# Kernel optimization log

Hardware: AMD Instinct MI355X
Metric: run time of the kernel (lower is better)

The kernel has to match this reference:

```python
import jax, jax.numpy as jnp
import numpy as np

N_NODES = 50000


def _gcn_conv(x, edge_index, W, b):
    """PyG-style GCNConv: add self-loops, symmetric deg^-1/2 norm, linear + scatter-add + bias."""
    n = x.shape[0]
    # add self loops
    loop = jnp.arange(n, dtype=edge_index.dtype)
    src = jnp.concatenate([edge_index[0], loop])  # [E+N]
    dst = jnp.concatenate([edge_index[1], loop])
    ones = jnp.ones_like(dst, dtype=x.dtype)
    deg = jax.ops.segment_sum(ones, dst, num_segments=n)  # in-degree incl. self loop
    deg_inv_sqrt = jnp.where(deg > 0, jax.lax.rsqrt(deg), 0.0)
    norm = deg_inv_sqrt[src] * deg_inv_sqrt[dst]  # [E+N]
    h = x @ W  # [N, out]
    msg = h[src] * norm[:, None]  # gather + scale, [E+N, out]
    out = jax.ops.segment_sum(msg, dst, num_segments=n)  # scatter-add
    return out + b


def setup_inputs() -> dict:
    key = jax.random.key(0)
    k1, k2, k3, k4 = jax.random.split(key, 4)
    in_ch, hid, z = 128, 128, 64
    x = jax.random.normal(k1, (N_NODES, in_ch), dtype=jnp.float32)
    edge_index = jax.random.randint(k2, (2, 800000), 0, N_NODES, dtype=jnp.int64)
    W1 = jax.random.normal(k3, (in_ch, hid), dtype=jnp.float32) * (1.0 / np.sqrt(in_ch))
    b1 = jnp.zeros((hid,), dtype=jnp.float32)
    W2 = jax.random.normal(k4, (hid, z), dtype=jnp.float32) * (1.0 / np.sqrt(hid))
    b2 = jnp.zeros((z,), dtype=jnp.float32)
    return {"x": x, "edge_index": edge_index, "W1": W1, "b1": b1, "W2": W2, "b2": b2}


def reference(x, edge_index, W1, b1, W2, b2):
    h = jax.nn.relu(_gcn_conv(x, edge_index, W1, b1))
    return _gcn_conv(h, edge_index, W2, b2)
```

## Files before the change

### kernel.cpp

```cpp
#include <hip/hip_runtime.h>

static constexpr int K = 128;
static constexpr int CAP = 8192;

using ushort8 = __attribute__((ext_vector_type(8))) unsigned short;
using bf16x8  = __attribute__((ext_vector_type(8))) __bf16;
using f32x4   = __attribute__((ext_vector_type(4))) float;

__device__ inline float bflo(unsigned u) { return __uint_as_float(u << 16); }
__device__ inline float bfhi(unsigned u) { return __uint_as_float(u & 0xFFFF0000u); }
__device__ inline unsigned short f2bf(float f) {
    unsigned u = __float_as_uint(f);
    return (unsigned short)((u + 0x7FFF + ((u >> 16) & 1)) >> 16);
}


__global__ __launch_bounds__(256) void k_bin(const int* __restrict__ ei, int e,
                                             int* __restrict__ gcur,
                                             unsigned long long* __restrict__ tmp) {
    constexpr int PER = 4;
    __shared__ int cnt[256], base[256], cur[256];
    int t = threadIdx.x;
    int chunk0 = blockIdx.x * 256 * PER;
    cnt[t] = 0;
    __syncthreads();
    int ds[PER];
#pragma unroll
    for (int k2 = 0; k2 < PER; ++k2) {
        int i = chunk0 + k2 * 256 + t;
        ds[k2] = (i < e) ? ei[(size_t)e + i] : -1;
        if (ds[k2] >= 0) atomicAdd(&cnt[ds[k2] >> 8], 1);
    }
    __syncthreads();
    int c = cnt[t];
    base[t] = c ? atomicAdd(&gcur[t], c) : 0;
    cur[t] = 0;
    __syncthreads();
#pragma unroll
    for (int k2 = 0; k2 < PER; ++k2) {
        int i = chunk0 + k2 * 256 + t;
        if (i < e) {
            int b = ds[k2] >> 8;
            int pos = base[b] + atomicAdd(&cur[b], 1);
            tmp[(size_t)b * CAP + pos] =
                ((unsigned long long)(unsigned)ds[k2] << 32) | (unsigned)ei[i];
        }
    }
}

__global__ __launch_bounds__(256) void k_bscan(const int* __restrict__ gcur,
                                               int* __restrict__ bbase,
                                               int nb, int* __restrict__ offs,
                                               int n, int e) {
    __shared__ int sh[256];
    int t = threadIdx.x;
    int v = (t < nb) ? gcur[t] : 0;
    sh[t] = v;
    __syncthreads();
    for (int o = 1; o < 256; o <<= 1) {
        int x = (t >= o) ? sh[t - o] : 0;
        __syncthreads();
        sh[t] += x;
        __syncthreads();
    }
    bbase[t] = sh[t] - v;
    if (t == 255) bbase[256] = sh[255];
    if (t == 0) offs[n] = e;
}

__global__ __launch_bounds__(1024) void k_csr(const unsigned long long* __restrict__ tmp,
                                              const int* __restrict__ bbase,
                                              int* __restrict__ offs,
                                              int* __restrict__ srt,
                                              float* __restrict__ dinv, int n) {
    __shared__ int cntS[256], sh[256], cur[256];
    int b = blockIdx.x;
    int t = threadIdx.x;
    int beg = bbase[b];
    int tot = bbase[b + 1] - beg;
    const unsigned long long* tb = tmp + (size_t)b * CAP;
    if (t < 256) cntS[t] = 0;
    __syncthreads();
    for (int i = t; i < tot; i += 1024)
        atomicAdd(&cntS[(int)(tb[i] >> 32) & 255], 1);
    __syncthreads();
    int v = (t < 256) ? cntS[t] : 0;
    if (t < 256) sh[t] = v;
    __syncthreads();
    for (int o = 1; o < 256; o <<= 1) {
        int x = (t < 256 && t >= o) ? sh[t - o] : 0;
        __syncthreads();
        if (t < 256) sh[t] += x;
        __syncthreads();
    }
    if (t < 256) {
        int pfx = sh[t] - v;
        int node = b * 256 + t;
        if (node < n) {
            offs[node] = beg + pfx;
            dinv[node] = rsqrtf((float)(v + 1));
        }
        cur[t] = pfx;
    }
    __syncthreads();
    for (int i = t; i < tot; i += 1024) {
        unsigned long long pr = tb[i];
        int d = (int)(pr >> 32);
        int pos = atomicAdd(&cur[d & 255], 1);
        srt[beg + pos] = (int)(pr & 0xFFFFFFFFu);
    }
}


template <int COUT>
__global__ __launch_bounds__(256) void k_gemm_mfma(const float* __restrict__ X,
                                                   const float* __restrict__ W,
                                                   const float* __restrict__ dinv,
                                                   unsigned short* __restrict__ G, int n) {
    constexpr int BM = 64, BK = 32;
    constexpr int NCT = COUT / 16;
    constexpr int NCH = K / BK;
    constexpr int WT = COUT * (BK / 8) / 256;
    __shared__ unsigned short Ah[BM * BK], Al[BM * BK];
    __shared__ unsigned short Bh[COUT * BK], Bl[COUT * BK];
    __shared__ float dS[BM];
    const int tid = threadIdx.x;
    const int row0 = blockIdx.x * BM;
    if (tid < BM) {
        int gr = row0 + tid;
        dS[tid] = (gr < n) ? dinv[gr] : 0.f;
    }

    float4 xr[2];
    float wr[WT][8];

    auto loadX = [&](int kc) {
        int r = tid >> 2, ks = tid & 3;
        int gr = row0 + r;
        if (gr < n) {
            const float4* pp = (const float4*)(X + (size_t)gr * K + kc * BK + ks * 8);
            xr[0] = pp[0];
            xr[1] = pp[1];
        } else {
            xr[0] = make_float4(0.f, 0.f, 0.f, 0.f);
            xr[1] = xr[0];
        }
    };
    auto loadW = [&](int kc) {
#pragma unroll
        for (int q = 0; q < WT; ++q) {
            int i = tid + q * 256;
            int c = i % COUT, ks = i / COUT;
#pragma unroll
            for (int j = 0; j < 8; ++j)
                wr[q][j] = W[(size_t)(kc * BK + ks * 8 + j) * COUT + c];
        }
    };
    auto storeLDS = [&]() {
        int r = tid >> 2, ks = tid & 3;
        ushort8 h, l;
        const float* f = (const float*)&xr[0];
#pragma unroll
        for (int j = 0; j < 8; ++j) {
            unsigned short hh = f2bf(f[j]);
            h[j] = hh;
            l[j] = f2bf(f[j] - __uint_as_float((unsigned)hh << 16));
        }
        *(ushort8*)&Ah[r * BK + ks * 8] = h;
        *(ushort8*)&Al[r * BK + ks * 8] = l;
#pragma unroll
        for (int q = 0; q < WT; ++q) {
            int i = tid + q * 256;
            int c = i % COUT, ks2 = i / COUT;
            ushort8 wh, wl;
#pragma unroll
            for (int j = 0; j < 8; ++j) {
                unsigned short hh = f2bf(wr[q][j]);
                wh[j] = hh;
                wl[j] = f2bf(wr[q][j] - __uint_as_float((unsigned)hh << 16));
            }
            *(ushort8*)&Bh[c * BK + ks2 * 8] = wh;
            *(ushort8*)&Bl[c * BK + ks2 * 8] = wl;
        }
    };

    f32x4 acc[NCT] = {};
    const int l = tid & 63, wv = tid >> 6;
    const int l16 = l & 15, lk = l >> 4;
    const int arow = wv * 16 + l16;

    loadX(0);
    loadW(0);
    storeLDS();
    __syncthreads();
    for (int c = 0; c < NCH; ++c) {
        if (c + 1 < NCH) { loadX(c + 1); loadW(c + 1); }
        bf16x8 ah = *(const bf16x8*)&Ah[arow * BK + lk * 8];
        bf16x8 al = *(const bf16x8*)&Al[arow * BK + lk * 8];
#pragma unroll
        for (int ct = 0; ct < NCT; ++ct) {
            bf16x8 bh = *(const bf16x8*)&Bh[(ct * 16 + l16) * BK + lk * 8];
            bf16x8 bl = *(const bf16x8*)&Bl[(ct * 16 + l16) * BK + lk * 8];
            acc[ct] = __builtin_amdgcn_mfma_f32_16x16x32_bf16(ah, bh, acc[ct], 0, 0, 0);
            acc[ct] = __builtin_amdgcn_mfma_f32_16x16x32_bf16(al, bh, acc[ct], 0, 0, 0);
            acc[ct] = __builtin_amdgcn_mfma_f32_16x16x32_bf16(ah, bl, acc[ct], 0, 0, 0);
        }
        if (c + 1 < NCH) {
            __syncthreads();
            storeLDS();
            __syncthreads();
        }
    }

#pragma unroll
    for (int ct = 0; ct < NCT; ++ct) {
        int col = ct * 16 + l16;
#pragma unroll
        for (int r4 = 0; r4 < 4; ++r4) {
            int lr = wv * 16 + lk * 4 + r4;
            int gr = row0 + lr;
            if (gr < n) G[(size_t)gr * COUT + col] = f2bf(acc[ct][r4] * dS[lr]);
        }
    }
}


__global__ __launch_bounds__(256) void k_gemm_bf16(const unsigned short* __restrict__ X,
                                                   const float* __restrict__ W,
                                                   const float* __restrict__ dinv,
                                                   unsigned short* __restrict__ G, int n) {
    constexpr int COUT = 64, BM = 64, BK = 32;
    constexpr int NCT = COUT / 16;
    constexpr int NCH = K / BK;
    __shared__ unsigned short Ah[BM * BK];
    __shared__ unsigned short Bh[COUT * BK], Bl[COUT * BK];
    __shared__ float dS[BM];
    const int tid = threadIdx.x;
    const int row0 = blockIdx.x * BM;
    if (tid < BM) {
        int gr = row0 + tid;
        dS[tid] = (gr < n) ? dinv[gr] : 0.f;
    }

    ushort8 xrb;
    float wr[8];

    auto loadX = [&](int kc) {
        int r = tid >> 2, ks = tid & 3;
        int gr = row0 + r;
        if (gr < n)
            xrb = *(const ushort8*)(X + (size_t)gr * K + kc * BK + ks * 8);
        else
            xrb = (ushort8){0, 0, 0, 0, 0, 0, 0, 0};
    };
    auto loadW = [&](int kc) {
        int c = tid % COUT, ks = tid / COUT;
#pragma unroll
        for (int j = 0; j < 8; ++j)
            wr[j] = W[(size_t)(kc * BK + ks * 8 + j) * COUT + c];
    };
    auto storeLDS = [&]() {
        int r = tid >> 2, ks = tid & 3;
        *(ushort8*)&Ah[r * BK + ks * 8] = xrb;
        int c = tid % COUT, ks2 = tid / COUT;
        ushort8 wh, wl;
#pragma unroll
        for (int j = 0; j < 8; ++j) {
            unsigned short hh = f2bf(wr[j]);
            wh[j] = hh;
            wl[j] = f2bf(wr[j] - __uint_as_float((unsigned)hh << 16));
        }
        *(ushort8*)&Bh[c * BK + ks2 * 8] = wh;
        *(ushort8*)&Bl[c * BK + ks2 * 8] = wl;
    };

    f32x4 acc[NCT] = {};
    const int l = tid & 63, wv = tid >> 6;
    const int l16 = l & 15, lk = l >> 4;
    const int arow = wv * 16 + l16;

    loadX(0);
    loadW(0);
    storeLDS();
    __syncthreads();
    for (int c = 0; c < NCH; ++c) {
        if (c + 1 < NCH) { loadX(c + 1); loadW(c + 1); }
        bf16x8 ah = *(const bf16x8*)&Ah[arow * BK + lk * 8];
#pragma unroll
        for (int ct = 0; ct < NCT; ++ct) {
            bf16x8 bh = *(const bf16x8*)&Bh[(ct * 16 + l16) * BK + lk * 8];
            bf16x8 bl = *(const bf16x8*)&Bl[(ct * 16 + l16) * BK + lk * 8];
            acc[ct] = __builtin_amdgcn_mfma_f32_16x16x32_bf16(ah, bh, acc[ct], 0, 0, 0);
            acc[ct] = __builtin_amdgcn_mfma_f32_16x16x32_bf16(ah, bl, acc[ct], 0, 0, 0);
        }
        if (c + 1 < NCH) {
            __syncthreads();
            storeLDS();
            __syncthreads();
        }
    }

#pragma unroll
    for (int ct = 0; ct < NCT; ++ct) {
        int col = ct * 16 + l16;
#pragma unroll
        for (int r4 = 0; r4 < 4; ++r4) {
            int lr = wv * 16 + lk * 4 + r4;
            int gr = row0 + lr;
            if (gr < n) G[(size_t)gr * COUT + col] = f2bf(acc[ct][r4] * dS[lr]);
        }
    }
}


#define ADD8(u)                                      \
    do {                                             \
        a[0] += bflo((u).x); a[1] += bfhi((u).x);    \
        a[2] += bflo((u).y); a[3] += bfhi((u).y);    \
        a[4] += bflo((u).z); a[5] += bfhi((u).z);    \
        a[6] += bflo((u).w); a[7] += bfhi((u).w);    \
    } while (0)

__global__ __launch_bounds__(256) void k_reduce128(const int* __restrict__ offs,
                                                   const int* __restrict__ srt,
                                                   const uint4* __restrict__ g4,
                                                   const float* __restrict__ dinv,
                                                   const float* __restrict__ bias,
                                                   unsigned short* __restrict__ out, int n) {
    int node = blockIdx.x * 4 + (threadIdx.x >> 6);
    if (node >= n) return;
    int lane = threadIdx.x & 63;
    int l16 = lane & 15, grp = lane >> 4;
    int beg = offs[node], end = offs[node + 1];

    float a[8] = {};
    if (grp == 0) {
        uint4 u = g4[(size_t)node * 16 + l16];
        ADD8(u);
    }
    int j = beg + grp;
    for (; j + 12 < end; j += 16) {
        uint4 u0 = g4[(size_t)srt[j]      * 16 + l16];
        uint4 u1 = g4[(size_t)srt[j + 4]  * 16 + l16];
        uint4 u2 = g4[(size_t)srt[j + 8]  * 16 + l16];
        uint4 u3 = g4[(size_t)srt[j + 12] * 16 + l16];
        ADD8(u0); ADD8(u1); ADD8(u2); ADD8(u3);
    }
    for (; j < end; j += 4) {
        uint4 u = g4[(size_t)srt[j] * 16 + l16];
        ADD8(u);
    }
#pragma unroll
    for (int q = 0; q < 8; ++q) {
        a[q] += __shfl_xor(a[q], 16);
        a[q] += __shfl_xor(a[q], 32);
    }
    if (lane < 16) {
        float di = dinv[node];
        ushort8 o;
#pragma unroll
        for (int q = 0; q < 8; ++q) {
            float v = fmaf(di, a[q], bias[l16 * 8 + q]);
            o[q] = f2bf(fmaxf(v, 0.f));
        }
        *(ushort8*)(out + (size_t)node * 128 + l16 * 8) = o;
    }
}

__global__ __launch_bounds__(256) void k_reduce64(const int* __restrict__ offs,
                                                  const int* __restrict__ srt,
                                                  const uint4* __restrict__ g4,
                                                  const float* __restrict__ dinv,
                                                  const float* __restrict__ bias,
                                                  float* __restrict__ out, int n) {
    int node = blockIdx.x * 4 + (threadIdx.x >> 6);
    if (node >= n) return;
    int lane = threadIdx.x & 63;
    int l8 = lane & 7, grp = lane >> 3;
    int beg = offs[node], end = offs[node + 1];

    float a[8] = {};
    if (grp == 0) {
        uint4 u = g4[(size_t)node * 8 + l8];
        ADD8(u);
    }
    int j = beg + grp;
    for (; j + 8 < end; j += 16) {
        uint4 u0 = g4[(size_t)srt[j]     * 8 + l8];
        uint4 u1 = g4[(size_t)srt[j + 8] * 8 + l8];
        ADD8(u0); ADD8(u1);
    }
    for (; j < end; j += 8) {
        uint4 u = g4[(size_t)srt[j] * 8 + l8];
        ADD8(u);
    }
#pragma unroll
    for (int q = 0; q < 8; ++q) {
        a[q] += __shfl_xor(a[q], 8);
        a[q] += __shfl_xor(a[q], 16);
        a[q] += __shfl_xor(a[q], 32);
    }
    if (lane < 8) {
        float di = dinv[node];
        float4 b0 = ((const float4*)bias)[l8 * 2];
        float4 b1 = ((const float4*)bias)[l8 * 2 + 1];
        float4 o0, o1;
        o0.x = fmaf(di, a[0], b0.x); o0.y = fmaf(di, a[1], b0.y);
        o0.z = fmaf(di, a[2], b0.z); o0.w = fmaf(di, a[3], b0.w);
        o1.x = fmaf(di, a[4], b1.x); o1.y = fmaf(di, a[5], b1.y);
        o1.z = fmaf(di, a[6], b1.z); o1.w = fmaf(di, a[7], b1.w);
        float4* op = (float4*)(out + (size_t)node * 64 + l8 * 8);
        op[0] = o0;
        op[1] = o1;
    }
}

extern "C" void kernel_launch(void* const* d_in, const int* in_sizes, int n_in,
                              void* d_out, int out_size, void* d_ws, size_t ws_size,
                              hipStream_t stream) {
    const float* x  = (const float*)d_in[0];
    const int*   ei = (const int*)d_in[1];
    const float* W1 = (const float*)d_in[2];
    const float* b1 = (const float*)d_in[3];
    const float* W2 = (const float*)d_in[4];
    const float* b2 = (const float*)d_in[5];
    float* out = (float*)d_out;

    const int n = in_sizes[0] / K;
    const int e = in_sizes[1] / 2;
    const int nb = (n + 255) / 256;

    char* p = (char*)d_ws;
    unsigned long long* tmp = (unsigned long long*)p;  p += (size_t)nb * CAP * 8;
    int* gcur  = (int*)p;  p += 256 * 4;
    int* bbase = (int*)p;  p += 257 * 4;
    int* offs  = (int*)p;  p += (size_t)(n + 1) * 4;
    int* srt   = (int*)p;  p += (size_t)e * 4;
    float* dinv = (float*)p;  p += (size_t)n * 4;
    p = (char*)(((uintptr_t)p + 15) & ~(uintptr_t)15);
    unsigned short* G1 = (unsigned short*)p;  p += (size_t)n * 128 * 2;
    p = (char*)(((uintptr_t)p + 15) & ~(uintptr_t)15);
    unsigned short* H = (unsigned short*)p;   p += (size_t)n * 128 * 2;
    p = (char*)(((uintptr_t)p + 15) & ~(uintptr_t)15);
    unsigned short* G2 = (unsigned short*)p;

    hipMemsetAsync(gcur, 0, 256 * sizeof(int), stream);
    k_bin<<<(e + 1023) / 1024, 256, 0, stream>>>(ei, e, gcur, tmp);
    k_bscan<<<1, 256, 0, stream>>>(gcur, bbase, nb, offs, n, e);
    k_csr<<<nb, 1024, 0, stream>>>(tmp, bbase, offs, srt, dinv, n);

    k_gemm_mfma<128><<<(n + 63) / 64, 256, 0, stream>>>(x, W1, dinv, G1, n);
    k_reduce128<<<(n + 3) / 4, 256, 0, stream>>>(offs, srt, (const uint4*)G1,
                                                 dinv, b1, H, n);

    k_gemm_bf16<<<(n + 63) / 64, 256, 0, stream>>>(H, W2, dinv, G2, n);
    k_reduce64<<<(n + 3) / 4, 256, 0, stream>>>(offs, srt, (const uint4*)G2,
                                                dinv, b2, out, n);
}
```

Before: 135.0 us.

## Fold bucket scan into CSR kernel, register-cache edges, drop weight low-split MFMAs

New measurement: 129.9 us. 1.04x faster.

```diff
diff --git a/kernel.cpp b/kernel.cpp
--- a/kernel.cpp
+++ b/kernel.cpp
@@ -48,41 +48,38 @@
     }
 }
 
-__global__ __launch_bounds__(256) void k_bscan(const int* __restrict__ gcur,
-                                               int* __restrict__ bbase,
-                                               int nb, int* __restrict__ offs,
-                                               int n, int e) {
-    __shared__ int sh[256];
-    int t = threadIdx.x;
-    int v = (t < nb) ? gcur[t] : 0;
-    sh[t] = v;
-    __syncthreads();
-    for (int o = 1; o < 256; o <<= 1) {
-        int x = (t >= o) ? sh[t - o] : 0;
-        __syncthreads();
-        sh[t] += x;
-        __syncthreads();
-    }
-    bbase[t] = sh[t] - v;
-    if (t == 255) bbase[256] = sh[255];
-    if (t == 0) offs[n] = e;
-}
-
 __global__ __launch_bounds__(1024) void k_csr(const unsigned long long* __restrict__ tmp,
-                                              const int* __restrict__ bbase,
+                                              const int* __restrict__ gcur,
                                               int* __restrict__ offs,
                                               int* __restrict__ srt,
-                                              float* __restrict__ dinv, int n) {
-    __shared__ int cntS[256], sh[256], cur[256];
-    int b = blockIdx.x;
-    int t = threadIdx.x;
-    int beg = bbase[b];
-    int tot = bbase[b + 1] - beg;
+                                              float* __restrict__ dinv, int n, int e) {
+    __shared__ int cntS[256], sh[256], cur[256], bsum[256];
+    const int b = blockIdx.x;
+    const int t = threadIdx.x;
+    const int tot = gcur[b];
     const unsigned long long* tb = tmp + (size_t)b * CAP;
+
+    unsigned long long pr[8];
+#pragma unroll
+    for (int p = 0; p < 8; ++p) {
+        int i = t + p * 1024;
+        pr[p] = (i < tot) ? tb[i] : 0;
+    }
+
+    if (t < 256) bsum[t] = (t < b) ? gcur[t] : 0;
     if (t < 256) cntS[t] = 0;
     __syncthreads();
-    for (int i = t; i < tot; i += 1024)
-        atomicAdd(&cntS[(int)(tb[i] >> 32) & 255], 1);
+    for (int o = 128; o > 0; o >>= 1) {
+        if (t < o) bsum[t] += bsum[t + o];
+        __syncthreads();
+    }
+    const int beg = bsum[0];
+
+#pragma unroll
+    for (int p = 0; p < 8; ++p) {
+        int i = t + p * 1024;
+        if (i < tot) atomicAdd(&cntS[(int)(pr[p] >> 32) & 255], 1);
+    }
     __syncthreads();
     int v = (t < 256) ? cntS[t] : 0;
     if (t < 256) sh[t] = v;
@@ -102,12 +99,16 @@
         }
         cur[t] = pfx;
     }
-    __syncthreads();
-    for (int i = t; i < tot; i += 1024) {
-        unsigned long long pr = tb[i];
-        int d = (int)(pr >> 32);
-        int pos = atomicAdd(&cur[d & 255], 1);
-        srt[beg + pos] = (int)(pr & 0xFFFFFFFFu);
+    if (b == (int)gridDim.x - 1 && t == 0) offs[n] = e;
+    __syncthreads();
+#pragma unroll
+    for (int p = 0; p < 8; ++p) {
+        int i = t + p * 1024;
+        if (i < tot) {
+            int d = (int)(pr[p] >> 32);
+            int pos = atomicAdd(&cur[d & 255], 1);
+            srt[beg + pos] = (int)(pr[p] & 0xFFFFFFFFu);
+        }
     }
 }
 
@@ -122,7 +123,7 @@
     constexpr int NCH = K / BK;
     constexpr int WT = COUT * (BK / 8) / 256;
     __shared__ unsigned short Ah[BM * BK], Al[BM * BK];
-    __shared__ unsigned short Bh[COUT * BK], Bl[COUT * BK];
+    __shared__ unsigned short Bh[COUT * BK];
     __shared__ float dS[BM];
     const int tid = threadIdx.x;
     const int row0 = blockIdx.x * BM;
@@ -172,15 +173,10 @@
         for (int q = 0; q < WT; ++q) {
             int i = tid + q * 256;
             int c = i % COUT, ks2 = i / COUT;
-            ushort8 wh, wl;
-#pragma unroll
-            for (int j = 0; j < 8; ++j) {
-                unsigned short hh = f2bf(wr[q][j]);
-                wh[j] = hh;
-                wl[j] = f2bf(wr[q][j] - __uint_as_float((unsigned)hh << 16));
-            }
+            ushort8 wh;
+#pragma unroll
+            for (int j = 0; j < 8; ++j) wh[j] = f2bf(wr[q][j]);
             *(ushort8*)&Bh[c * BK + ks2 * 8] = wh;
-            *(ushort8*)&Bl[c * BK + ks2 * 8] = wl;
         }
     };
 
@@ -200,10 +196,8 @@
 #pragma unroll
         for (int ct = 0; ct < NCT; ++ct) {
             bf16x8 bh = *(const bf16x8*)&Bh[(ct * 16 + l16) * BK + lk * 8];
-            bf16x8 bl = *(const bf16x8*)&Bl[(ct * 16 + l16) * BK + lk * 8];
             acc[ct] = __builtin_amdgcn_mfma_f32_16x16x32_bf16(ah, bh, acc[ct], 0, 0, 0);
             acc[ct] = __builtin_amdgcn_mfma_f32_16x16x32_bf16(al, bh, acc[ct], 0, 0, 0);
-            acc[ct] = __builtin_amdgcn_mfma_f32_16x16x32_bf16(ah, bl, acc[ct], 0, 0, 0);
         }
         if (c + 1 < NCH) {
             __syncthreads();
@@ -233,7 +227,7 @@
     constexpr int NCT = COUT / 16;
     constexpr int NCH = K / BK;
     __shared__ unsigned short Ah[BM * BK];
-    __shared__ unsigned short Bh[COUT * BK], Bl[COUT * BK];
+    __shared__ unsigned short Bh[COUT * BK];
     __shared__ float dS[BM];
     const int tid = threadIdx.x;
     const int row0 = blockIdx.x * BM;
@@ -263,15 +257,10 @@
         int r = tid >> 2, ks = tid & 3;
         *(ushort8*)&Ah[r * BK + ks * 8] = xrb;
         int c = tid % COUT, ks2 = tid / COUT;
-        ushort8 wh, wl;
-#pragma unroll
-        for (int j = 0; j < 8; ++j) {
-            unsigned short hh = f2bf(wr[j]);
-            wh[j] = hh;
-            wl[j] = f2bf(wr[j] - __uint_as_float((unsigned)hh << 16));
-        }
+        ushort8 wh;
+#pragma unroll
+        for (int j = 0; j < 8; ++j) wh[j] = f2bf(wr[j]);
         *(ushort8*)&Bh[c * BK + ks2 * 8] = wh;
-        *(ushort8*)&Bl[c * BK + ks2 * 8] = wl;
     };
 
     f32x4 acc[NCT] = {};
@@ -289,9 +278,7 @@
 #pragma unroll
         for (int ct = 0; ct < NCT; ++ct) {
             bf16x8 bh = *(const bf16x8*)&Bh[(ct * 16 + l16) * BK + lk * 8];
-            bf16x8 bl = *(const bf16x8*)&Bl[(ct * 16 + l16) * BK + lk * 8];
             acc[ct] = __builtin_amdgcn_mfma_f32_16x16x32_bf16(ah, bh, acc[ct], 0, 0, 0);
-            acc[ct] = __builtin_amdgcn_mfma_f32_16x16x32_bf16(ah, bl, acc[ct], 0, 0, 0);
         }
         if (c + 1 < NCH) {
             __syncthreads();
@@ -433,7 +420,6 @@
     char* p = (char*)d_ws;
     unsigned long long* tmp = (unsigned long long*)p;  p += (size_t)nb * CAP * 8;
     int* gcur  = (int*)p;  p += 256 * 4;
-    int* bbase = (int*)p;  p += 257 * 4;
     int* offs  = (int*)p;  p += (size_t)(n + 1) * 4;
     int* srt   = (int*)p;  p += (size_t)e * 4;
     float* dinv = (float*)p;  p += (size_t)n * 4;
@@ -446,8 +432,7 @@
 
     hipMemsetAsync(gcur, 0, 256 * sizeof(int), stream);
     k_bin<<<(e + 1023) / 1024, 256, 0, stream>>>(ei, e, gcur, tmp);
-    k_bscan<<<1, 256, 0, stream>>>(gcur, bbase, nb, offs, n, e);
-    k_csr<<<nb, 1024, 0, stream>>>(tmp, bbase, offs, srt, dinv, n);
+    k_csr<<<nb, 1024, 0, stream>>>(tmp, gcur, offs, srt, dinv, n, e);
 
     k_gemm_mfma<128><<<(n + 63) / 64, 256, 0, stream>>>(x, W1, dinv, G1, n);
     k_reduce128<<<(n + 3) / 4, 256, 0, stream>>>(offs, srt, (const uint4*)G1,
```
